# Kernel tuning notes

Measured on AMD Instinct MI355X. Metric: run time of the kernel, lower is better.

Reference implementation:

```python
import math
import jax, jax.numpy as jnp
import numpy as np

DIM = 4096
N_HEADS = 32
N_KV_HEADS = 8
HEAD_DIM = DIM // N_HEADS          # 128
N_REP = N_HEADS // N_KV_HEADS      # 4
B, T = 2, 2048
MAX_SEQ = 2048
ROPE_THETA = 500000.0


def _rope_tables(seq_len, head_dim, theta):
    inv = 1.0 / (theta ** (np.arange(0, head_dim, 2, dtype=np.float32) / head_dim))
    t = np.arange(seq_len, dtype=np.float32)
    ang = np.outer(t, inv)                      # [T, head_dim/2]
    return jnp.asarray(np.cos(ang)), jnp.asarray(np.sin(ang))


def setup_inputs() -> dict:
    key = jax.random.key(0)
    ks = jax.random.split(key, 6)
    scale = 0.02
    x = jax.random.normal(ks[0], (B, T, DIM), dtype=jnp.float32)
    wq = jax.random.normal(ks[1], (N_HEADS * HEAD_DIM, DIM), dtype=jnp.float32) * scale
    wk = jax.random.normal(ks[2], (N_KV_HEADS * HEAD_DIM, DIM), dtype=jnp.float32) * scale
    wv = jax.random.normal(ks[3], (N_KV_HEADS * HEAD_DIM, DIM), dtype=jnp.float32) * scale
    wo = jax.random.normal(ks[4], (DIM, N_HEADS * HEAD_DIM), dtype=jnp.float32) * scale
    freqs_cos, freqs_sin = _rope_tables(T, HEAD_DIM, ROPE_THETA)
    cache_k = jnp.zeros((B, MAX_SEQ, N_KV_HEADS, HEAD_DIM), dtype=jnp.float32)
    cache_v = jnp.zeros((B, MAX_SEQ, N_KV_HEADS, HEAD_DIM), dtype=jnp.float32)
    mask = jnp.zeros((T, T), dtype=jnp.float32)  # NOTE: unused by the original forward
    return {"x": x, "wq": wq, "wk": wk, "wv": wv, "wo": wo,
            "freqs_cos": freqs_cos, "freqs_sin": freqs_sin,
            "cache_k": cache_k, "cache_v": cache_v,
            "mask": mask, "start_pos": 0}


def _apply_rope(t, cos, sin):
    # t: [B, T, H, hd]; even/odd interleaved pairs form complex numbers
    tr = t.reshape(*t.shape[:-1], HEAD_DIM // 2, 2)
    xr, xi = tr[..., 0], tr[..., 1]
    c = cos[None, :, None, :]
    s = sin[None, :, None, :]
    out_r = xr * c - xi * s
    out_i = xr * s + xi * c
    return jnp.stack([out_r, out_i], axis=-1).reshape(t.shape)


def reference(x, wq, wk, wv, wo, freqs_cos, freqs_sin, cache_k, cache_v, mask, start_pos):
    Bx, Tx, _ = x.shape
    q = (x @ wq.T).reshape(Bx, Tx, N_HEADS, HEAD_DIM)
    k = (x @ wk.T).reshape(Bx, Tx, N_KV_HEADS, HEAD_DIM)
    v = (x @ wv.T).reshape(Bx, Tx, N_KV_HEADS, HEAD_DIM)

    q = _apply_rope(q, freqs_cos, freqs_sin)
    k = _apply_rope(k, freqs_cos, freqs_sin)

    # KV-cache append (start_pos is a static Python int)
    cache_k = jax.lax.dynamic_update_slice(cache_k, k, (0, start_pos, 0, 0))
    cache_v = jax.lax.dynamic_update_slice(cache_v, v, (0, start_pos, 0, 0))
    S = start_pos + Tx

    # GQA expansion via torch-style .repeat (tiling: head h -> kv head h % n_kv)
    keys = jnp.tile(cache_k[:, :S], (1, 1, N_REP, 1))    # [B, S, H, hd]
    values = jnp.tile(cache_v[:, :S], (1, 1, N_REP, 1))  # [B, S, H, hd]

    scores = jnp.einsum('bthd,bshd->bhts', q, keys) / math.sqrt(HEAD_DIM)
    # NOTE: the original forward never adds `mask` — faithful unmasked softmax
    probs = jax.nn.softmax(scores, axis=-1)
    ctx = jnp.einsum('bhts,bshd->bthd', probs, values).reshape(Bx, Tx, N_HEADS * HEAD_DIM)
    return ctx @ wo.T
```

## Files before the change

kernel.cpp:

```cpp
#include <hip/hip_runtime.h>
#include <hip/hip_bf16.h>
#include <cstdint>


typedef short bf16x8 __attribute__((ext_vector_type(8)));
typedef float f32x4  __attribute__((ext_vector_type(4)));

__device__ __forceinline__ float b2f(unsigned short h) {
  union { uint32_t u; float f; } v; v.u = ((uint32_t)h) << 16; return v.f;
}
__device__ __forceinline__ unsigned short f2b(float f) {
  union { float f; uint32_t u; } v; v.f = f;
  uint32_t r = (v.u + 0x7FFFu + ((v.u >> 16) & 1u)) >> 16;
  return (unsigned short)r;
}
__device__ __forceinline__ uint32_t cvt_pk_bf16(float lo, float hi) {
  uint32_t r;
  asm("v_cvt_pk_bf16_f32 %0, %1, %2" : "=v"(r) : "v"(lo), "v"(hi));
  return r;
}
__device__ __forceinline__ float lo2f(uint32_t u) {
  union { uint32_t u; float f; } w; w.u = u << 16; return w.f;
}
__device__ __forceinline__ float hi2f(uint32_t u) {
  union { uint32_t u; float f; } w; w.u = u & 0xffff0000u; return w.f;
}

#define GLDS16(gp, lp)                                                        \
  __builtin_amdgcn_global_load_lds(                                           \
      (const __attribute__((address_space(1))) unsigned int*)(gp),            \
      (__attribute__((address_space(3))) unsigned int*)(lp), 16, 0, 0)

__global__ __launch_bounds__(256) void cast_f32_bf16(
    const float* __restrict__ in, unsigned short* __restrict__ out, int n4) {
  int i = blockIdx.x * 256 + threadIdx.x;
  if (i < n4) {
    float4 v = ((const float4*)in)[i];
    ushort4 o;
    o.x = f2b(v.x); o.y = f2b(v.y); o.z = f2b(v.z); o.w = f2b(v.w);
    ((ushort4*)out)[i] = o;
  }
}

__device__ __forceinline__ void stout(float* p, float v) { *p = v; }
__device__ __forceinline__ void stout(unsigned short* p, float v) { *p = f2b(v); }

template <typename OUT>
__global__ __launch_bounds__(256, 2) void gemm_bt(
    const unsigned short* __restrict__ A, const unsigned short* __restrict__ B,
    OUT* __restrict__ C, int M, int N, int K) {
  __shared__ __align__(16) unsigned short As[128][64];
  __shared__ __align__(16) unsigned short Bs[128][64];

  const int tid  = threadIdx.x;
  const int lane = tid & 63;
  const int wave = tid >> 6;
  const int col  = lane & 15;
  const int quad = lane >> 4;
  const int bm = blockIdx.y * 128;
  const int bn = blockIdx.x * 128;
  const int wm = (wave & 1) * 64;
  const int wn = (wave >> 1) * 64;

  f32x4 acc[4][4];
#pragma unroll
  for (int i = 0; i < 4; ++i)
#pragma unroll
    for (int j = 0; j < 4; ++j) acc[i][j] = (f32x4){0.f, 0.f, 0.f, 0.f};

  const int srow0  = tid >> 3;
  const int gchunk = (tid & 7) ^ ((tid >> 3) & 7);
  const unsigned short* Ag = A + (size_t)(bm + srow0) * K + gchunk * 8;
  const unsigned short* Bg = B + (size_t)(bn + srow0) * K + gchunk * 8;
  unsigned short* Al = &As[0][0] + tid * 8;
  unsigned short* Bl = &Bs[0][0] + tid * 8;

  for (int k0 = 0; k0 < K; k0 += 64) {
    __syncthreads();
#pragma unroll
    for (int r = 0; r < 4; ++r) {
      GLDS16(Ag + k0 + (size_t)r * 32 * K, Al + r * 2048);
      GLDS16(Bg + k0 + (size_t)r * 32 * K, Bl + r * 2048);
    }
    __syncthreads();
#pragma unroll
    for (int ks = 0; ks < 2; ++ks) {
      bf16x8 a[4], b[4];
      const int slot = ((ks * 4 + quad) ^ (col & 7)) * 8;
#pragma unroll
      for (int i = 0; i < 4; ++i)
        a[i] = *(const bf16x8*)&As[wm + i * 16 + col][slot];
#pragma unroll
      for (int j = 0; j < 4; ++j)
        b[j] = *(const bf16x8*)&Bs[wn + j * 16 + col][slot];
#pragma unroll
      for (int i = 0; i < 4; ++i)
#pragma unroll
        for (int j = 0; j < 4; ++j)
          acc[i][j] = __builtin_amdgcn_mfma_f32_16x16x32_bf16(a[i], b[j],
                                                              acc[i][j], 0, 0, 0);
    }
  }

#pragma unroll
  for (int i = 0; i < 4; ++i) {
    int row = bm + wm + i * 16 + quad * 4;
#pragma unroll
    for (int j = 0; j < 4; ++j) {
      int cc = bn + wn + j * 16 + col;
#pragma unroll
      for (int r2 = 0; r2 < 4; ++r2)
        stout(C + (size_t)(row + r2) * N + cc, acc[i][j][r2]);
    }
  }
}

__global__ __launch_bounds__(256) void rope_qk(
    unsigned short* __restrict__ qkv, const float* __restrict__ cosT,
    const float* __restrict__ sinT) {
  int idx = blockIdx.x * 256 + threadIdx.x;
  int m = idx / 640;
  int p = idx - m * 640;
  int head = p >> 4, i4 = p & 15;
  int t = m & 2047;
  unsigned short* ptr = qkv + (size_t)m * 6144 + head * 128 + i4 * 8;
  uint4 v = *(const uint4*)ptr;
  float4 c = *(const float4*)&cosT[t * 64 + i4 * 4];
  float4 s = *(const float4*)&sinT[t * 64 + i4 * 4];
  float x0 = lo2f(v.x), y0 = hi2f(v.x);
  float x1 = lo2f(v.y), y1 = hi2f(v.y);
  float x2 = lo2f(v.z), y2 = hi2f(v.z);
  float x3 = lo2f(v.w), y3 = hi2f(v.w);
  uint4 o;
  o.x = cvt_pk_bf16(x0 * c.x - y0 * s.x, x0 * s.x + y0 * c.x);
  o.y = cvt_pk_bf16(x1 * c.y - y1 * s.y, x1 * s.y + y1 * c.y);
  o.z = cvt_pk_bf16(x2 * c.z - y2 * s.z, x2 * s.z + y2 * c.z);
  o.w = cvt_pk_bf16(x3 * c.w - y3 * s.w, x3 * s.w + y3 * c.w);
  *(uint4*)ptr = o;
}

__global__ __launch_bounds__(256) void transpose_v(
    const unsigned short* __restrict__ qkv, unsigned short* __restrict__ vt) {
  __shared__ unsigned short tile[64][72];
  int b = blockIdx.z >> 3, kvh = blockIdx.z & 7;
  int s0 = blockIdx.x * 64, d0 = blockIdx.y * 64;
  int tc = threadIdx.x & 63, tr = threadIdx.x >> 6;
#pragma unroll
  for (int r = 0; r < 16; ++r) {
    int row = r * 4 + tr;
    tile[row][tc] =
        qkv[(size_t)(b * 2048 + s0 + row) * 6144 + 5120 + kvh * 128 + d0 + tc];
  }
  __syncthreads();
#pragma unroll
  for (int r = 0; r < 16; ++r) {
    int drow = r * 4 + tr;
    vt[(size_t)((b * 8 + kvh) * 128 + d0 + drow) * 2048 + s0 + tc] =
        tile[tc][drow];
  }
}

__global__ __launch_bounds__(256, 2) void attn(
    const unsigned short* __restrict__ qkv, const unsigned short* __restrict__ vt,
    unsigned short* __restrict__ ctx) {
  constexpr int T = 2048, LD = 6144;
  const int qt = blockIdx.x, h = blockIdx.y, b = blockIdx.z;
  const int kvh = h & 7;
  const int tid = threadIdx.x, lane = tid & 63, wave = tid >> 6;
  const int col = lane & 15, quad = lane >> 4;

  __shared__ __align__(1024) char smem[40960];
  auto Qs = (unsigned short(*)[128][8])smem;
  auto Ks = (unsigned short(*)[128])smem;
  auto Vs = (unsigned short(*)[64])(smem + 16384);
  auto Ps = (unsigned short(*)[64])(smem + 32768);

  {
    const int row = tid & 127, kc0 = tid >> 7;
    const unsigned short* g =
        qkv + (size_t)(b * T + qt * 128 + row) * LD + h * 128 + kc0 * 8;
    unsigned short* l = &Qs[kc0][row][0];
#pragma unroll
    for (int r = 0; r < 8; ++r) GLDS16(g + r * 16, l + r * 2048);
  }
  __syncthreads();

  bf16x8 qf[2][4];
#pragma unroll
  for (int mi = 0; mi < 2; ++mi)
#pragma unroll
    for (int ks = 0; ks < 4; ++ks)
      qf[mi][ks] = *(const bf16x8*)&Qs[ks * 4 + quad][wave * 32 + mi * 16 + col][0];

  float mrow[2], lrow[2];
  f32x4 oacc[2][8];
#pragma unroll
  for (int mi = 0; mi < 2; ++mi) { mrow[mi] = -1e30f; lrow[mi] = 0.f; }
#pragma unroll
  for (int mi = 0; mi < 2; ++mi)
#pragma unroll
    for (int d = 0; d < 8; ++d) oacc[mi][d] = (f32x4){0.f, 0.f, 0.f, 0.f};

  const float scale = 0.08838834764831845f;
  const float l2e = 1.4426950408889634f;
  const float c1 = scale * l2e;

  const int krow0 = tid >> 4;
  const int kgch  = (tid & 15) ^ ((tid >> 4) & 15);
  const int vrow0 = tid >> 3;
  const int vgch  = (tid & 7) ^ ((tid >> 3) & 7);
  unsigned short* Klin = &Ks[0][0] + tid * 8;
  unsigned short* Vlin = &Vs[0][0] + tid * 8;

  const int rq  = wave * 16 + col;
  const int c14 = col & 14;

  for (int s0 = 0; s0 < T; s0 += 64) {
    __syncthreads();
    {
      const unsigned short* g =
          qkv + (size_t)(b * T + s0 + krow0) * LD + 4096 + kvh * 128 + kgch * 8;
#pragma unroll
      for (int r = 0; r < 4; ++r)
        GLDS16(g + (size_t)r * 16 * LD, Klin + r * 2048);
      const unsigned short* gv =
          vt + (size_t)((b * 8 + kvh) * 128 + vrow0) * T + s0 + vgch * 8;
#pragma unroll
      for (int r = 0; r < 4; ++r)
        GLDS16(gv + (size_t)r * 32 * T, Vlin + r * 2048);
    }
    __syncthreads();

    f32x4 sacc[2][4];
#pragma unroll
    for (int mi = 0; mi < 2; ++mi)
#pragma unroll
      for (int j = 0; j < 4; ++j) sacc[mi][j] = (f32x4){0.f, 0.f, 0.f, 0.f};
#pragma unroll
    for (int ks = 0; ks < 4; ++ks) {
      bf16x8 ak[4];
#pragma unroll
      for (int j = 0; j < 4; ++j)
        ak[j] = *(const bf16x8*)&Ks[j * 16 + col][((ks * 4 + quad) ^ col) * 8];
#pragma unroll
      for (int mi = 0; mi < 2; ++mi)
#pragma unroll
        for (int j = 0; j < 4; ++j)
          sacc[mi][j] = __builtin_amdgcn_mfma_f32_16x16x32_bf16(
              ak[j], qf[mi][ks], sacc[mi][j], 0, 0, 0);
    }

    bf16x8 bp[2][2];
#pragma unroll
    for (int mi = 0; mi < 2; ++mi) {
      float mx = sacc[mi][0][0];
#pragma unroll
      for (int j = 0; j < 4; ++j)
#pragma unroll
        for (int r = 0; r < 4; ++r) mx = fmaxf(mx, sacc[mi][j][r]);
      mx = fmaxf(mx, __shfl_xor(mx, 16));
      mx = fmaxf(mx, __shfl_xor(mx, 32));
      mx *= scale;
      float mold = mrow[mi];
      float mnew = fmaxf(mold, mx);
      float alpha = exp2f((mold - mnew) * l2e);
      mrow[mi] = mnew;
      const float mml = mnew * l2e;
      float rsum = 0.f;
#pragma unroll
      for (int j = 0; j < 4; ++j) {
        float p0 = exp2f(sacc[mi][j][0] * c1 - mml);
        float p1 = exp2f(sacc[mi][j][1] * c1 - mml);
        float p2 = exp2f(sacc[mi][j][2] * c1 - mml);
        float p3 = exp2f(sacc[mi][j][3] * c1 - mml);
        rsum += (p0 + p1) + (p2 + p3);
        uint2 pk;
        pk.x = cvt_pk_bf16(p0, p1);
        pk.y = cvt_pk_bf16(p2, p3);
        const int ws = (j * 4 + quad) ^ c14;
        *(uint2*)&Ps[rq][ws * 4] = pk;
      }
      bp[mi][0] = *(const bf16x8*)&Ps[rq][((quad * 2) ^ c14) * 4];
      bp[mi][1] = *(const bf16x8*)&Ps[rq][((8 + quad * 2) ^ c14) * 4];
      rsum += __shfl_xor(rsum, 16);
      rsum += __shfl_xor(rsum, 32);
      lrow[mi] = lrow[mi] * alpha + rsum;
#pragma unroll
      for (int di = 0; di < 8; ++di) {
#pragma unroll
        for (int r = 0; r < 4; ++r) oacc[mi][di][r] *= alpha;
      }
    }

#pragma unroll
    for (int ks = 0; ks < 2; ++ks) {
#pragma unroll
      for (int di = 0; di < 8; ++di) {
        bf16x8 va = *(const bf16x8*)
            &Vs[di * 16 + col][(((ks * 4 + quad) ^ (col & 7))) * 8];
#pragma unroll
        for (int mi = 0; mi < 2; ++mi)
          oacc[mi][di] = __builtin_amdgcn_mfma_f32_16x16x32_bf16(
              va, bp[mi][ks], oacc[mi][di], 0, 0, 0);
      }
    }
  }

#pragma unroll
  for (int mi = 0; mi < 2; ++mi) {
    float inv = 1.0f / lrow[mi];
    int row = qt * 128 + wave * 32 + mi * 16 + col;
    unsigned short* cp = ctx + (size_t)(b * T + row) * 4096 + h * 128;
#pragma unroll
    for (int di = 0; di < 8; ++di) {
      uint2 o;
      o.x = cvt_pk_bf16(oacc[mi][di][0] * inv, oacc[mi][di][1] * inv);
      o.y = cvt_pk_bf16(oacc[mi][di][2] * inv, oacc[mi][di][3] * inv);
      *(uint2*)(cp + di * 16 + quad * 4) = o;
    }
  }
}

extern "C" void kernel_launch(void* const* d_in, const int* in_sizes, int n_in,
                              void* d_out, int out_size, void* d_ws,
                              size_t ws_size, hipStream_t stream) {
  const float* x  = (const float*)d_in[0];
  const float* wq = (const float*)d_in[1];
  const float* wk = (const float*)d_in[2];
  const float* wv = (const float*)d_in[3];
  const float* wo = (const float*)d_in[4];
  const float* fc = (const float*)d_in[5];
  const float* fs = (const float*)d_in[6];
  float* out = (float*)d_out;

  char* ws = (char*)d_ws;
  unsigned short* xb  = (unsigned short*)(ws);
  unsigned short* wb  = (unsigned short*)(ws + 33554432);
  unsigned short* qkv = (unsigned short*)(ws + 33554432 + 50331648);
  unsigned short* vtp = (unsigned short*)(ws + 33554432 + 50331648 + 50331648);

  cast_f32_bf16<<<16384, 256, 0, stream>>>(x, xb, 4194304);
  cast_f32_bf16<<<16384, 256, 0, stream>>>(wq, wb, 4194304);
  cast_f32_bf16<<<4096, 256, 0, stream>>>(wk, wb + 16777216, 1048576);
  cast_f32_bf16<<<4096, 256, 0, stream>>>(wv, wb + 20971520, 1048576);

  dim3 g1(48, 32);
  gemm_bt<unsigned short><<<g1, 256, 0, stream>>>(xb, wb, qkv, 4096, 6144, 4096);

  cast_f32_bf16<<<16384, 256, 0, stream>>>(wo, wb, 4194304);

  rope_qk<<<10240, 256, 0, stream>>>(qkv, fc, fs);

  dim3 g2(32, 2, 16);
  transpose_v<<<g2, 256, 0, stream>>>(qkv, vtp);

  dim3 g3(16, 32, 2);
  attn<<<g3, 256, 0, stream>>>(qkv, vtp, xb);

  dim3 g4(32, 32);
  gemm_bt<float><<<g4, 256, 0, stream>>>(xb, wb, out, 4096, 4096, 4096);
}
```

Measured before the change: 815.8 us.

## Prefetch next K/V tiles in attention loop and use v_max3 for row max

```diff
diff --git a/kernel.cpp b/kernel.cpp
--- a/kernel.cpp
+++ b/kernel.cpp
@@ -24,6 +24,11 @@
 }
 __device__ __forceinline__ float hi2f(uint32_t u) {
   union { uint32_t u; float f; } w; w.u = u & 0xffff0000u; return w.f;
+}
+__device__ __forceinline__ float max3f(float a, float b, float c) {
+  float r;
+  asm("v_max3_f32 %0, %1, %2, %3" : "=v"(r) : "v"(a), "v"(b), "v"(c));
+  return r;
 }
 
 #define GLDS16(gp, lp)                                                        \
@@ -191,6 +196,7 @@
 #pragma unroll
     for (int ks = 0; ks < 4; ++ks)
       qf[mi][ks] = *(const bf16x8*)&Qs[ks * 4 + quad][wave * 32 + mi * 16 + col][0];
+  __syncthreads();
 
   float mrow[2], lrow[2];
   f32x4 oacc[2][8];
@@ -211,26 +217,21 @@
   const int vgch  = (tid & 7) ^ ((tid >> 3) & 7);
   unsigned short* Klin = &Ks[0][0] + tid * 8;
   unsigned short* Vlin = &Vs[0][0] + tid * 8;
+  const unsigned short* Kg0 =
+      qkv + (size_t)(b * T + krow0) * LD + 4096 + kvh * 128 + kgch * 8;
+  const unsigned short* Vg0 =
+      vt + (size_t)((b * 8 + kvh) * 128 + vrow0) * T + vgch * 8;
 
   const int rq  = wave * 16 + col;
   const int c14 = col & 14;
 
+#pragma unroll
+  for (int r = 0; r < 4; ++r) GLDS16(Kg0 + (size_t)r * 16 * LD, Klin + r * 2048);
+#pragma unroll
+  for (int r = 0; r < 4; ++r) GLDS16(Vg0 + (size_t)r * 32 * T, Vlin + r * 2048);
+  __syncthreads();
+
   for (int s0 = 0; s0 < T; s0 += 64) {
-    __syncthreads();
-    {
-      const unsigned short* g =
-          qkv + (size_t)(b * T + s0 + krow0) * LD + 4096 + kvh * 128 + kgch * 8;
-#pragma unroll
-      for (int r = 0; r < 4; ++r)
-        GLDS16(g + (size_t)r * 16 * LD, Klin + r * 2048);
-      const unsigned short* gv =
-          vt + (size_t)((b * 8 + kvh) * 128 + vrow0) * T + s0 + vgch * 8;
-#pragma unroll
-      for (int r = 0; r < 4; ++r)
-        GLDS16(gv + (size_t)r * 32 * T, Vlin + r * 2048);
-    }
-    __syncthreads();
-
     f32x4 sacc[2][4];
 #pragma unroll
     for (int mi = 0; mi < 2; ++mi)
@@ -250,14 +251,23 @@
               ak[j], qf[mi][ks], sacc[mi][j], 0, 0, 0);
     }
 
+    __syncthreads();
+    if (s0 + 64 < T) {
+      const unsigned short* g = Kg0 + (size_t)(s0 + 64) * LD;
+#pragma unroll
+      for (int r = 0; r < 4; ++r)
+        GLDS16(g + (size_t)r * 16 * LD, Klin + r * 2048);
+    }
+
     bf16x8 bp[2][2];
 #pragma unroll
     for (int mi = 0; mi < 2; ++mi) {
-      float mx = sacc[mi][0][0];
-#pragma unroll
-      for (int j = 0; j < 4; ++j)
-#pragma unroll
-        for (int r = 0; r < 4; ++r) mx = fmaxf(mx, sacc[mi][j][r]);
+      float m0 = max3f(sacc[mi][0][0], sacc[mi][0][1], sacc[mi][0][2]);
+      float m1 = max3f(sacc[mi][0][3], sacc[mi][1][0], sacc[mi][1][1]);
+      float m2 = max3f(sacc[mi][1][2], sacc[mi][1][3], sacc[mi][2][0]);
+      float m3 = max3f(sacc[mi][2][1], sacc[mi][2][2], sacc[mi][2][3]);
+      float m4 = max3f(sacc[mi][3][0], sacc[mi][3][1], sacc[mi][3][2]);
+      float mx = max3f(max3f(m0, m1, m2), fmaxf(m3, m4), sacc[mi][3][3]);
       mx = fmaxf(mx, __shfl_xor(mx, 16));
       mx = fmaxf(mx, __shfl_xor(mx, 32));
       mx *= scale;
@@ -304,6 +314,14 @@
               va, bp[mi][ks], oacc[mi][di], 0, 0, 0);
       }
     }
+
+    __syncthreads();
+    if (s0 + 64 < T) {
+      const unsigned short* gv = Vg0 + (s0 + 64);
+#pragma unroll
+      for (int r = 0; r < 4; ++r)
+        GLDS16(gv + (size_t)r * 32 * T, Vlin + r * 2048);
+    }
   }
 
 #pragma unroll
```

Result: slower. 844.1 us (+3.5%).
